# Kernel optimization log

Hardware: AMD Instinct MI355X
Metric: run time of the kernel (lower is better)

Reference implementation:

```python
import jax, jax.numpy as jnp
import numpy as np

D = 1024
H = 16
DK = D // H  # 64
CHUNK = 64
EPS = 1e-5


def setup_inputs() -> dict:
    key = jax.random.key(0)
    k1, k2, k3 = jax.random.split(key, 3)
    x = jax.random.normal(k1, (4, 4096, D), dtype=jnp.float32)
    W_qkv = jax.random.normal(k2, (D, 3 * D), dtype=jnp.float32) * 0.02
    W_o = jax.random.normal(k3, (D, D), dtype=jnp.float32) * 0.02
    return {"x": x, "W_qkv": W_qkv, "W_o": W_o}


def _layernorm_noaffine(k):
    mu = jnp.mean(k, axis=-1, keepdims=True)
    var = jnp.mean((k - mu) ** 2, axis=-1, keepdims=True)  # biased var, torch LayerNorm
    return (k - mu) / jnp.sqrt(var + EPS)


def _linear_attn(x, W_qkv, W_o):
    B, L, Dm = x.shape
    qkv = (x @ W_qkv).reshape(B, L, 3, H, DK)
    q, k, v = qkv[:, :, 0], qkv[:, :, 1], qkv[:, :, 2]
    k = _layernorm_noaffine(k)

    nC = L // CHUNK
    # [nC, B, C, H, DK] for scan over chunks
    to_chunks = lambda t: t.reshape(B, nC, CHUNK, H, DK).transpose(1, 0, 2, 3, 4)
    qc, kc, vc = to_chunks(q), to_chunks(k), to_chunks(v)

    causal = jnp.tril(jnp.ones((CHUNK, CHUNK), dtype=bool))  # s <= t inclusive

    def step(S, chunk):
        q_c, k_c, v_c = chunk  # each [B, C, H, DK]
        # inter-chunk: y_t += S_prev @ q_t
        inter = jnp.einsum('bhde,bthe->bthd', S, q_c)
        # intra-chunk: y_t += sum_{s<=t} (k_s . q_t) v_s
        scores = jnp.einsum('bthd,bshd->bhts', q_c, k_c)
        scores = jnp.where(causal, scores, 0.0)
        intra = jnp.einsum('bhts,bshd->bthd', scores, v_c)
        # state update: S += sum_t v_t k_t^T
        S = S + jnp.einsum('bthd,bthe->bhde', v_c, k_c)
        return S, inter + intra

    S0 = jnp.zeros((B, H, DK, DK), dtype=x.dtype)
    _, ys = jax.lax.scan(step, S0, (qc, kc, vc))  # ys: [nC, B, C, H, DK]
    y = ys.transpose(1, 0, 2, 3, 4).reshape(B, L, Dm)
    return y @ W_o


def reference(x, W_qkv, W_o):
    return _linear_attn(x, W_qkv, W_o)
```

## Files before the change

kernel.cpp:

```cpp
#include <hip/hip_runtime.h>

#define EPS 1e-5f

typedef __attribute__((ext_vector_type(8))) short s16x8;
typedef __attribute__((ext_vector_type(4))) float f4;

__device__ __forceinline__ short f2bf(float f) {
  union { float f; unsigned u; } x; x.f = f;
  unsigned r = x.u + 0x7fffu + ((x.u >> 16) & 1u);
  return (short)(r >> 16);
}
__device__ __forceinline__ float bf2f(short s) {
  union { unsigned u; float f; } x; x.u = ((unsigned)(unsigned short)s) << 16;
  return x.f;
}
__device__ __forceinline__ void gll16(const short* g, short* l) {
  __builtin_amdgcn_global_load_lds((const __attribute__((address_space(1))) void*)g,
                                   (__attribute__((address_space(3))) void*)l, 16, 0, 0);
}

#define BAR() asm volatile("s_barrier" ::: "memory")
#define LGKM0() do { asm volatile("s_waitcnt lgkmcnt(0)" ::: "memory"); \
                     __builtin_amdgcn_sched_barrier(0); } while (0)

__global__ __launch_bounds__(256) void prep(
    const float* __restrict__ x, const float* __restrict__ Wqkv,
    const float* __restrict__ Wo,
    short* __restrict__ xb, short* __restrict__ WqkvT, short* __restrict__ WoT)
{
  __shared__ float tile[32][33];
  const int bid = blockIdx.x;
  if (bid < 8192) {
    const size_t i = ((size_t)bid * 256 + threadIdx.x) * 8;
    const float4* p = reinterpret_cast<const float4*>(x + i);
    float4 a = p[0], b = p[1];
    union { uint4 v; short s[8]; } o;
    o.s[0] = f2bf(a.x); o.s[1] = f2bf(a.y); o.s[2] = f2bf(a.z); o.s[3] = f2bf(a.w);
    o.s[4] = f2bf(b.x); o.s[5] = f2bf(b.y); o.s[6] = f2bf(b.z); o.s[7] = f2bf(b.w);
    *reinterpret_cast<uint4*>(xb + i) = o.v;
    return;
  }
  const float* W; short* WT; int K, N, t;
  if (bid < 11264) { W = Wqkv; WT = WqkvT; K = 1024; N = 3072; t = bid - 8192;  }
  else             { W = Wo;   WT = WoT;   K = 1024; N = 1024; t = bid - 11264; }
  const int nblk = N >> 5;
  const int n0 = (t % nblk) * 32, k0 = (t / nblk) * 32;
  const int tx = threadIdx.x & 31, ty = threadIdx.x >> 5;
  #pragma unroll
  for (int i = 0; i < 4; i++) {
    int r = ty + i * 8;
    tile[r][tx] = W[(size_t)(k0 + r) * N + n0 + tx];
  }
  __syncthreads();
  #pragma unroll
  for (int i = 0; i < 4; i++) {
    int r = ty + i * 8;
    WT[(size_t)(n0 + r) * K + k0 + tx] = f2bf(tile[tx][r]);
  }
}

__device__ __forceinline__ void stage_slice(const short* __restrict__ G, short* dstbase,
                                            int row0, int kcol, int rowgrp, int panel, int lane) {
  short* dst = dstbase + panel * 8192 + rowgrp * 512;
  const short* src = G + (size_t)(row0 + rowgrp * 16 + (lane >> 2)) * 1024
                       + kcol + panel * 32 + (((lane & 3) << 3) ^ ((lane >> 5) << 4));
  gll16(src, dst);
}

template<bool STAGE>
__device__ __forceinline__ void ktile8p(
    const short* ldsAc, const short* ldsBc, short* ldsAn, short* ldsBn,
    const short* __restrict__ A, const short* __restrict__ BT,
    int m0, int n0, int knext,
    int w, int lane, int wm, int wn, int quad, int l16,
    f4 (&acc)[8][4])
{
  s16x8 bfr[4][2];
  const int co = (quad << 3) ^ ((l16 >> 3) << 4);
  #pragma unroll
  for (int p = 0; p < 4; ++p) {
    s16x8 a00, a01, a10, a11;
    {
      const int r0 = (wm * 128 + p * 32 + l16) * 32;
      a00 = *reinterpret_cast<const s16x8*>(&ldsAc[r0 + co]);
      a01 = *reinterpret_cast<const s16x8*>(&ldsAc[8192 + r0 + co]);
      a10 = *reinterpret_cast<const s16x8*>(&ldsAc[r0 + 512 + co]);
      a11 = *reinterpret_cast<const s16x8*>(&ldsAc[8192 + r0 + 512 + co]);
    }
    if (p == 0) {
      #pragma unroll
      for (int nf = 0; nf < 4; ++nf) {
        const int rb = (wn * 64 + nf * 16 + l16) * 32;
        bfr[nf][0] = *reinterpret_cast<const s16x8*>(&ldsBc[rb + co]);
        bfr[nf][1] = *reinterpret_cast<const s16x8*>(&ldsBc[8192 + rb + co]);
      }
    }
    if (STAGE) {
      if (p == 0)      { stage_slice(BT, ldsBn, n0, knext, w,     0, lane); stage_slice(BT, ldsBn, n0, knext, w,     1, lane); }
      else if (p == 1) { stage_slice(BT, ldsBn, n0, knext, 8 + w, 0, lane); stage_slice(BT, ldsBn, n0, knext, 8 + w, 1, lane); }
      else if (p == 2) { const int rg = (w & 3) + ((w >> 2) << 3);
                         stage_slice(A, ldsAn, m0, knext, rg, 0, lane); stage_slice(A, ldsAn, m0, knext, rg, 1, lane); }
      else             { const int rg = 4 + (w & 3) + ((w >> 2) << 3);
                         stage_slice(A, ldsAn, m0, knext, rg, 0, lane); stage_slice(A, ldsAn, m0, knext, rg, 1, lane); }
    }
    BAR();
    LGKM0();
    __builtin_amdgcn_s_setprio(1);
    #pragma unroll
    for (int nf = 0; nf < 4; ++nf) {
      acc[2*p  ][nf] = __builtin_amdgcn_mfma_f32_16x16x32_bf16(a00, bfr[nf][0], acc[2*p  ][nf], 0, 0, 0);
      acc[2*p  ][nf] = __builtin_amdgcn_mfma_f32_16x16x32_bf16(a01, bfr[nf][1], acc[2*p  ][nf], 0, 0, 0);
      acc[2*p+1][nf] = __builtin_amdgcn_mfma_f32_16x16x32_bf16(a10, bfr[nf][0], acc[2*p+1][nf], 0, 0, 0);
      acc[2*p+1][nf] = __builtin_amdgcn_mfma_f32_16x16x32_bf16(a11, bfr[nf][1], acc[2*p+1][nf], 0, 0, 0);
    }
    __builtin_amdgcn_s_setprio(0);
    if (p == 1) {
      if (STAGE) asm volatile("s_waitcnt vmcnt(4)" ::: "memory");
      else       asm volatile("s_waitcnt vmcnt(0)" ::: "memory");
    }
    if (p == 3 && STAGE) asm volatile("s_waitcnt vmcnt(2)" ::: "memory");
    BAR();
  }
}

#define GEMM8P_PROLOGUE()                                                            \
  stage_slice(BT, Bb0, n0, 0, w,     0, lane); stage_slice(BT, Bb0, n0, 0, w,     1, lane); \
  stage_slice(BT, Bb0, n0, 0, 8 + w, 0, lane); stage_slice(BT, Bb0, n0, 0, 8 + w, 1, lane); \
  { const int rg = (w & 3) + ((w >> 2) << 3);                                        \
    stage_slice(A, Ab0, m0, 0, rg, 0, lane); stage_slice(A, Ab0, m0, 0, rg, 1, lane); } \
  { const int rg = 4 + (w & 3) + ((w >> 2) << 3);                                    \
    stage_slice(A, Ab0, m0, 0, rg, 0, lane); stage_slice(A, Ab0, m0, 0, rg, 1, lane); } \
  asm volatile("s_waitcnt vmcnt(2)" ::: "memory");                                   \
  BAR()

#define GEMM8P_MAINLOOP()                                                            \
  _Pragma("unroll 1")                                                                \
  for (int t = 0; t < 14; t += 2) {                                                  \
    ktile8p<true>(Ab0, Bb0, Ab1, Bb1, A, BT, m0, n0, (t + 1) << 6, w, lane, wm, wn, quad, l16, acc); \
    ktile8p<true>(Ab1, Bb1, Ab0, Bb0, A, BT, m0, n0, (t + 2) << 6, w, lane, wm, wn, quad, l16, acc); \
  }                                                                                  \
  ktile8p<true >(Ab0, Bb0, Ab1, Bb1, A, BT, m0, n0, 15 << 6, w, lane, wm, wn, quad, l16, acc); \
  ktile8p<false>(Ab1, Bb1, Ab0, Bb0, A, BT, m0, n0, 0,       w, lane, wm, wn, quad, l16, acc)

__global__ __launch_bounds__(512, 2) void gemm_qkv_8p(
    const short* __restrict__ A, const short* __restrict__ BT,
    short* __restrict__ qb, short* __restrict__ kb, short* __restrict__ vb)
{
  extern __shared__ __align__(16) short lds[];
  short* Ab0 = lds;           short* Ab1 = lds + 16384;
  short* Bb0 = lds + 32768;   short* Bb1 = lds + 49152;

  const int pid = blockIdx.x;
  const int wg = (pid & 7) * 96 + (pid >> 3);
  const int mb = wg / 12, nb = wg % 12;
  const int m0 = mb * 256, n0 = nb * 256;

  const int tid = threadIdx.x;
  const int w = tid >> 6, lane = tid & 63, quad = lane >> 4, l16 = lane & 15;
  const int wm = w >> 2, wn = w & 3;

  f4 acc[8][4];
  #pragma unroll
  for (int i = 0; i < 8; i++)
    #pragma unroll
    for (int j = 0; j < 4; j++) acc[i][j] = {0.f, 0.f, 0.f, 0.f};

  GEMM8P_PROLOGUE();
  GEMM8P_MAINLOOP();

  __syncthreads();
  short* st = lds + w * 1152;
  const int j0 = n0 + wn * 64;
  const int sq = j0 >> 10;
  const int hh = (j0 >> 6) & 15;
  short* dbuf = (sq == 0) ? qb : (sq == 1) ? kb : vb;
  const int r2 = lane >> 3, c8 = (lane & 7) << 3;
  #pragma unroll
  for (int mf = 0; mf < 8; ++mf) {
    #pragma unroll
    for (int nf = 0; nf < 4; ++nf)
      #pragma unroll
      for (int r = 0; r < 4; ++r)
        st[(quad * 4 + r) * 72 + nf * 16 + l16] = f2bf(acc[mf][nf][r]);
    #pragma unroll
    for (int h2 = 0; h2 < 2; ++h2) {
      int rr = h2 * 8 + r2;
      int i = m0 + wm * 128 + mf * 16 + rr;
      int bb = i >> 12, ll = i & 4095;
      uint4 val = *reinterpret_cast<const uint4*>(&st[rr * 72 + c8]);
      *reinterpret_cast<uint4*>(&dbuf[(((size_t)(bb * 16 + hh)) * 4096 + ll) * 64 + c8]) = val;
    }
  }
}

__global__ __launch_bounds__(512, 2) void gemm_out_8p(
    const short* __restrict__ A, const short* __restrict__ BT, float* __restrict__ C)
{
  extern __shared__ __align__(16) short lds[];
  short* Ab0 = lds;           short* Ab1 = lds + 16384;
  short* Bb0 = lds + 32768;   short* Bb1 = lds + 49152;

  const int pid = blockIdx.x;
  const int wg = (pid & 7) * 32 + (pid >> 3);
  const int mb = wg >> 2, nb = wg & 3;
  const int m0 = mb * 256, n0 = nb * 256;

  const int tid = threadIdx.x;
  const int w = tid >> 6, lane = tid & 63, quad = lane >> 4, l16 = lane & 15;
  const int wm = w >> 2, wn = w & 3;

  f4 acc[8][4];
  #pragma unroll
  for (int i = 0; i < 8; i++)
    #pragma unroll
    for (int j = 0; j < 4; j++) acc[i][j] = {0.f, 0.f, 0.f, 0.f};

  GEMM8P_PROLOGUE();
  GEMM8P_MAINLOOP();

  #pragma unroll
  for (int mf = 0; mf < 8; ++mf)
    #pragma unroll
    for (int nf = 0; nf < 4; ++nf)
      #pragma unroll
      for (int r = 0; r < 4; ++r) {
        int i = m0 + wm * 128 + mf * 16 + quad * 4 + r;
        int j = n0 + wn * 64 + nf * 16 + l16;
        C[(size_t)i * 1024 + j] = acc[mf][nf][r];
      }
}

__global__ __launch_bounds__(256) void gemm_qkv_v4(
    const short* __restrict__ A, const short* __restrict__ BT,
    short* __restrict__ qb, short* __restrict__ kb, short* __restrict__ vb)
{
  __shared__ __align__(16) short lds[8192];
  short* As = lds;
  short* Bs = lds + 4096;

  const int p = blockIdx.x;
  const int slot = p >> 3;
  const int strip = (p & 7) + 8 * (slot / 24);
  const int nb = slot % 24;
  const int m0 = strip * 128, n0 = nb * 128;

  const int tid = threadIdx.x;
  const int w = tid >> 6, lane = tid & 63, quad = lane >> 4, l16 = lane & 15;
  const int wm = (w >> 1) << 6, wn = (w & 1) << 6;

  f4 acc[4][4];
  #pragma unroll
  for (int i = 0; i < 4; i++)
    #pragma unroll
    for (int j = 0; j < 4; j++) acc[i][j] = {0.f, 0.f, 0.f, 0.f};

  const int row = w * 32 + (lane >> 2), ofs = (lane & 3) << 3;

  for (int k0 = 0; k0 < 1024; k0 += 32) {
    __syncthreads();
    gll16(A + (size_t)(m0 + row) * 1024 + k0 + ofs, &As[(w * 32) * 32]);
    gll16(A + (size_t)(m0 + row + 16) * 1024 + k0 + ofs, &As[(w * 32 + 16) * 32]);
    gll16(BT + (size_t)(n0 + row) * 1024 + k0 + ofs, &Bs[(w * 32) * 32]);
    gll16(BT + (size_t)(n0 + row + 16) * 1024 + k0 + ofs, &Bs[(w * 32 + 16) * 32]);
    __syncthreads();
    s16x8 afr[4], bfr[4];
    #pragma unroll
    for (int t = 0; t < 4; t++)
      afr[t] = *reinterpret_cast<const s16x8*>(&As[(wm + t * 16 + l16) * 32 + quad * 8]);
    #pragma unroll
    for (int t = 0; t < 4; t++)
      bfr[t] = *reinterpret_cast<const s16x8*>(&Bs[(wn + t * 16 + l16) * 32 + quad * 8]);
    #pragma unroll
    for (int ti = 0; ti < 4; ti++)
      #pragma unroll
      for (int tj = 0; tj < 4; tj++)
        acc[ti][tj] = __builtin_amdgcn_mfma_f32_16x16x32_bf16(afr[ti], bfr[tj], acc[ti][tj], 0, 0, 0);
  }

  __syncthreads();
  short* st = &lds[w * 16 * 72];
  const int j0 = n0 + wn;
  const int sq = j0 >> 10;
  const int hh = (j0 >> 6) & 15;
  short* dbuf = (sq == 0) ? qb : (sq == 1) ? kb : vb;
  const int r2 = lane >> 3, c8 = (lane & 7) << 3;
  #pragma unroll
  for (int ti = 0; ti < 4; ti++) {
    #pragma unroll
    for (int tj = 0; tj < 4; tj++)
      #pragma unroll
      for (int r = 0; r < 4; r++)
        st[(quad * 4 + r) * 72 + tj * 16 + l16] = f2bf(acc[ti][tj][r]);
    #pragma unroll
    for (int h2 = 0; h2 < 2; h2++) {
      int rr = h2 * 8 + r2;
      int i = m0 + wm + ti * 16 + rr;
      int bb = i >> 12, ll = i & 4095;
      uint4 val = *reinterpret_cast<const uint4*>(&st[rr * 72 + c8]);
      *reinterpret_cast<uint4*>(&dbuf[(((size_t)(bb * 16 + hh)) * 4096 + ll) * 64 + c8]) = val;
    }
  }
}

__global__ __launch_bounds__(256) void ln_k(short* __restrict__ kbuf)
{
  const int row = blockIdx.x * 4 + (threadIdx.x >> 6);
  const int lane = threadIdx.x & 63;
  const size_t idx = (size_t)row * 64 + lane;
  float v = bf2f(kbuf[idx]);
  float s = v, s2 = v * v;
  #pragma unroll
  for (int off = 32; off; off >>= 1) {
    s += __shfl_xor(s, off);
    s2 += __shfl_xor(s2, off);
  }
  float mean = s * (1.f / 64.f);
  float var = s2 * (1.f / 64.f) - mean * mean;
  float rstd = rsqrtf(var + EPS);
  kbuf[idx] = f2bf((v - mean) * rstd);
}

__global__ __launch_bounds__(256) void chunk_outer(
    const short* __restrict__ kb, const short* __restrict__ vb,
    short* __restrict__ G)
{
  __shared__ __align__(16) short kT[64 * 72];
  __shared__ __align__(16) short vT[64 * 72];
  const int bh = blockIdx.x >> 6, c = blockIdx.x & 63;
  const int tid = threadIdx.x;
  const int w = tid >> 6, lane = tid & 63, quad = lane >> 4, l16 = lane & 15;
  const int srow = tid >> 2, sseg = (tid & 3) << 4;
  const size_t base = (size_t)bh * 262144 + (size_t)(c * 64 + srow) * 64 + sseg;

  {
    const float4* kp = reinterpret_cast<const float4*>(kb + base);
    union { float4 v[2]; short s[16]; } ku;
    ku.v[0] = kp[0]; ku.v[1] = kp[1];
    float kv[16]; float s = 0.f, s2 = 0.f;
    #pragma unroll
    for (int i = 0; i < 16; i++) { kv[i] = bf2f(ku.s[i]); s += kv[i]; s2 += kv[i] * kv[i]; }
    s += __shfl_xor(s, 1);  s2 += __shfl_xor(s2, 1);
    s += __shfl_xor(s, 2);  s2 += __shfl_xor(s2, 2);
    float mean = s * (1.f / 64.f);
    float var = s2 * (1.f / 64.f) - mean * mean;
    float rstd = rsqrtf(var + EPS);
    #pragma unroll
    for (int i = 0; i < 16; i++) kT[(sseg + i) * 72 + srow] = f2bf((kv[i] - mean) * rstd);
    const float4* vp = reinterpret_cast<const float4*>(vb + base);
    union { float4 v[2]; short s[16]; } vu;
    vu.v[0] = vp[0]; vu.v[1] = vp[1];
    #pragma unroll
    for (int i = 0; i < 16; i++) vT[(sseg + i) * 72 + srow] = vu.s[i];
  }
  __syncthreads();
  s16x8 va0 = *reinterpret_cast<const s16x8*>(&vT[(w * 16 + l16) * 72 + quad * 8]);
  s16x8 va1 = *reinterpret_cast<const s16x8*>(&vT[(w * 16 + l16) * 72 + 32 + quad * 8]);
  short* Gc = G + ((size_t)blockIdx.x) * 4096;
  #pragma unroll
  for (int tj = 0; tj < 4; tj++) {
    s16x8 kb0 = *reinterpret_cast<const s16x8*>(&kT[(tj * 16 + l16) * 72 + quad * 8]);
    s16x8 kb1 = *reinterpret_cast<const s16x8*>(&kT[(tj * 16 + l16) * 72 + 32 + quad * 8]);
    f4 z = {0.f, 0.f, 0.f, 0.f};
    z = __builtin_amdgcn_mfma_f32_16x16x32_bf16(va0, kb0, z, 0, 0, 0);
    z = __builtin_amdgcn_mfma_f32_16x16x32_bf16(va1, kb1, z, 0, 0, 0);
    #pragma unroll
    for (int r = 0; r < 4; r++)
      Gc[(w * 16 + quad * 4 + r) * 64 + tj * 16 + l16] = f2bf(z[r]);
  }
}

__global__ __launch_bounds__(128) void prefix_S(short* __restrict__ G)
{
  const int bh = blockIdx.x >> 3, rg = blockIdx.x & 7;
  const size_t base = (size_t)bh * 262144 + rg * 512 + threadIdx.x * 4;
  float s0 = 0.f, s1 = 0.f, s2 = 0.f, s3 = 0.f;
  for (int c = 0; c < 64; c++) {
    short* p = G + base + (size_t)c * 4096;
    union { uint2 v; short s[4]; } gu;
    gu.v = *reinterpret_cast<const uint2*>(p);
    float g0 = bf2f(gu.s[0]), g1 = bf2f(gu.s[1]), g2 = bf2f(gu.s[2]), g3 = bf2f(gu.s[3]);
    union { uint2 v; short s[4]; } su;
    su.s[0] = f2bf(s0); su.s[1] = f2bf(s1); su.s[2] = f2bf(s2); su.s[3] = f2bf(s3);
    *reinterpret_cast<uint2*>(p) = su.v;
    s0 += g0; s1 += g1; s2 += g2; s3 += g3;
  }
}

__global__ __launch_bounds__(256) void chunk_out(
    const short* __restrict__ qb, const short* __restrict__ kb,
    const short* __restrict__ vb, const short* __restrict__ S,
    short* __restrict__ yb)
{
  __shared__ __align__(16) short vT[64 * 72];
  __shared__ __align__(16) short Ps[64 * 72];
  const int bh = blockIdx.x >> 6, c = blockIdx.x & 63;
  const int b = bh >> 4, h = bh & 15;
  const int tid = threadIdx.x;
  const int w = tid >> 6, lane = tid & 63, quad = lane >> 4, l16 = lane & 15;
  const int srow = tid >> 2, sseg = (tid & 3) << 4;
  const size_t base = (size_t)bh * 262144 + (size_t)c * 4096;

  {
    const float4* vp = reinterpret_cast<const float4*>(vb + base + (size_t)srow * 64 + sseg);
    union { float4 v[2]; short s[16]; } vu;
    vu.v[0] = vp[0]; vu.v[1] = vp[1];
    #pragma unroll
    for (int i = 0; i < 16; i++) vT[(sseg + i) * 72 + srow] = vu.s[i];
  }
  s16x8 qa[4][2], kf[2], sf[2];
  #pragma unroll
  for (int ti = 0; ti < 4; ti++)
    #pragma unroll
    for (int kh = 0; kh < 2; kh++)
      qa[ti][kh] = *reinterpret_cast<const s16x8*>(
          qb + base + (size_t)(ti * 16 + l16) * 64 + kh * 32 + quad * 8);
  #pragma unroll
  for (int kh = 0; kh < 2; kh++) {
    kf[kh] = *reinterpret_cast<const s16x8*>(
        kb + base + (size_t)(w * 16 + l16) * 64 + kh * 32 + quad * 8);
    sf[kh] = *reinterpret_cast<const s16x8*>(
        S + base + (size_t)(w * 16 + l16) * 64 + kh * 32 + quad * 8);
  }
  {
    float kv[16]; float s = 0.f, s2 = 0.f;
    #pragma unroll
    for (int kh = 0; kh < 2; kh++)
      #pragma unroll
      for (int i = 0; i < 8; i++) {
        float f = bf2f(kf[kh][i]); kv[kh * 8 + i] = f; s += f; s2 += f * f;
      }
    s += __shfl_xor(s, 16);  s2 += __shfl_xor(s2, 16);
    s += __shfl_xor(s, 32);  s2 += __shfl_xor(s2, 32);
    float mean = s * (1.f / 64.f);
    float var = s2 * (1.f / 64.f) - mean * mean;
    float rstd = rsqrtf(var + EPS);
    #pragma unroll
    for (int kh = 0; kh < 2; kh++)
      #pragma unroll
      for (int i = 0; i < 8; i++)
        kf[kh][i] = f2bf((kv[kh * 8 + i] - mean) * rstd);
  }
  __syncthreads();
  #pragma unroll
  for (int ti = 0; ti < 4; ti++) {
    f4 z = {0.f, 0.f, 0.f, 0.f};
    z = __builtin_amdgcn_mfma_f32_16x16x32_bf16(qa[ti][0], kf[0], z, 0, 0, 0);
    z = __builtin_amdgcn_mfma_f32_16x16x32_bf16(qa[ti][1], kf[1], z, 0, 0, 0);
    #pragma unroll
    for (int r = 0; r < 4; r++) {
      int t = ti * 16 + quad * 4 + r;
      int s = w * 16 + l16;
      Ps[t * 72 + s] = (s <= t) ? f2bf(z[r]) : (short)0;
    }
  }
  __syncthreads();
  s16x8 vf0 = *reinterpret_cast<const s16x8*>(&vT[(w * 16 + l16) * 72 + quad * 8]);
  s16x8 vf1 = *reinterpret_cast<const s16x8*>(&vT[(w * 16 + l16) * 72 + 32 + quad * 8]);
  #pragma unroll
  for (int ti = 0; ti < 4; ti++) {
    f4 z = {0.f, 0.f, 0.f, 0.f};
    s16x8 p0 = *reinterpret_cast<const s16x8*>(&Ps[(ti * 16 + l16) * 72 + quad * 8]);
    s16x8 p1 = *reinterpret_cast<const s16x8*>(&Ps[(ti * 16 + l16) * 72 + 32 + quad * 8]);
    z = __builtin_amdgcn_mfma_f32_16x16x32_bf16(p0, vf0, z, 0, 0, 0);
    z = __builtin_amdgcn_mfma_f32_16x16x32_bf16(p1, vf1, z, 0, 0, 0);
    z = __builtin_amdgcn_mfma_f32_16x16x32_bf16(qa[ti][0], sf[0], z, 0, 0, 0);
    z = __builtin_amdgcn_mfma_f32_16x16x32_bf16(qa[ti][1], sf[1], z, 0, 0, 0);
    #pragma unroll
    for (int r = 0; r < 4; r++) {
      int t = ti * 16 + quad * 4 + r;
      int d = w * 16 + l16;
      yb[(((size_t)b * 4096) + c * 64 + t) * 1024 + h * 64 + d] = f2bf(z[r]);
    }
  }
}

__global__ __launch_bounds__(256) void gemm_out_v3(
    const short* __restrict__ A, const short* __restrict__ BT, float* __restrict__ C)
{
  __shared__ __align__(16) short As[128 * 32];
  __shared__ __align__(16) short Bs[128 * 32];
  const int p = blockIdx.x;
  const int slot = p >> 3;
  const int strip = (p & 7) + 8 * (slot >> 3);
  const int nb = slot & 7;
  const int m0 = strip * 128, n0 = nb * 128;
  const int tid = threadIdx.x;
  const int w = tid >> 6, lane = tid & 63, quad = lane >> 4, l16 = lane & 15;
  const int wm = (w >> 1) << 6, wn = (w & 1) << 6;

  f4 acc[4][4];
  #pragma unroll
  for (int i = 0; i < 4; i++)
    #pragma unroll
    for (int j = 0; j < 4; j++) acc[i][j] = {0.f, 0.f, 0.f, 0.f};

  const int row = w * 32 + (lane >> 2), ofs = (lane & 3) << 3;

  for (int k0 = 0; k0 < 1024; k0 += 32) {
    __syncthreads();
    gll16(A + (size_t)(m0 + row) * 1024 + k0 + ofs, &As[(w * 32) * 32]);
    gll16(A + (size_t)(m0 + row + 16) * 1024 + k0 + ofs, &As[(w * 32 + 16) * 32]);
    gll16(BT + (size_t)(n0 + row) * 1024 + k0 + ofs, &Bs[(w * 32) * 32]);
    gll16(BT + (size_t)(n0 + row + 16) * 1024 + k0 + ofs, &Bs[(w * 32 + 16) * 32]);
    __syncthreads();
    s16x8 afr[4], bfr[4];
    #pragma unroll
    for (int t = 0; t < 4; t++)
      afr[t] = *reinterpret_cast<const s16x8*>(&As[(wm + t * 16 + l16) * 32 + quad * 8]);
    #pragma unroll
    for (int t = 0; t < 4; t++)
      bfr[t] = *reinterpret_cast<const s16x8*>(&Bs[(wn + t * 16 + l16) * 32 + quad * 8]);
    #pragma unroll
    for (int ti = 0; ti < 4; ti++)
      #pragma unroll
      for (int tj = 0; tj < 4; tj++)
        acc[ti][tj] = __builtin_amdgcn_mfma_f32_16x16x32_bf16(afr[ti], bfr[tj], acc[ti][tj], 0, 0, 0);
  }
  #pragma unroll
  for (int ti = 0; ti < 4; ti++)
    #pragma unroll
    for (int tj = 0; tj < 4; tj++)
      #pragma unroll
      for (int r = 0; r < 4; r++) {
        int i = m0 + wm + ti * 16 + quad * 4 + r;
        int j = n0 + wn + tj * 16 + l16;
        C[(size_t)i * 1024 + j] = acc[ti][tj][r];
      }
}

__global__ __launch_bounds__(256) void gemm_qkv_r1(
    const float* __restrict__ A, const float* __restrict__ B,
    short* __restrict__ qb, short* __restrict__ kb, short* __restrict__ vb)
{
  __shared__ __align__(16) short As[128 * 40];
  __shared__ __align__(16) short Bs[128 * 40];
  const int n0 = blockIdx.x * 128;
  const int m0 = blockIdx.y * 128;
  const int tid = threadIdx.x;
  const int w = tid >> 6, lane = tid & 63, quad = lane >> 4, l16 = lane & 15;
  const int wm = (w >> 1) << 6, wn = (w & 1) << 6;
  f4 acc[4][4];
  #pragma unroll
  for (int i = 0; i < 4; i++)
    #pragma unroll
    for (int j = 0; j < 4; j++) acc[i][j] = {0.f, 0.f, 0.f, 0.f};
  const int arow = tid >> 1, aseg = (tid & 1) << 4;
  const int brow = tid >> 3, bseg = (tid & 7) << 4;
  for (int k0 = 0; k0 < 1024; k0 += 32) {
    __syncthreads();
    {
      const float4* ap = reinterpret_cast<const float4*>(A + (size_t)(m0 + arow) * 1024 + k0 + aseg);
      union { float4 v[4]; float f[16]; } af;
      af.v[0] = ap[0]; af.v[1] = ap[1]; af.v[2] = ap[2]; af.v[3] = ap[3];
      union { float4 v[2]; short s[16]; } ao;
      #pragma unroll
      for (int i = 0; i < 16; i++) ao.s[i] = f2bf(af.f[i]);
      float4* dst = reinterpret_cast<float4*>(&As[arow * 40 + aseg]);
      dst[0] = ao.v[0]; dst[1] = ao.v[1];
    }
    {
      const float4* bp = reinterpret_cast<const float4*>(B + (size_t)(k0 + brow) * 3072 + n0 + bseg);
      union { float4 v[4]; float f[16]; } bu;
      bu.v[0] = bp[0]; bu.v[1] = bp[1]; bu.v[2] = bp[2]; bu.v[3] = bp[3];
      #pragma unroll
      for (int i = 0; i < 16; i++) Bs[(bseg + i) * 40 + brow] = f2bf(bu.f[i]);
    }
    __syncthreads();
    s16x8 afr[4], bfr[4];
    #pragma unroll
    for (int t = 0; t < 4; t++)
      afr[t] = *reinterpret_cast<const s16x8*>(&As[(wm + t * 16 + l16) * 40 + quad * 8]);
    #pragma unroll
    for (int t = 0; t < 4; t++)
      bfr[t] = *reinterpret_cast<const s16x8*>(&Bs[(wn + t * 16 + l16) * 40 + quad * 8]);
    #pragma unroll
    for (int ti = 0; ti < 4; ti++)
      #pragma unroll
      for (int tj = 0; tj < 4; tj++)
        acc[ti][tj] = __builtin_amdgcn_mfma_f32_16x16x32_bf16(afr[ti], bfr[tj], acc[ti][tj], 0, 0, 0);
  }
  const int sq = n0 >> 10;
  short* dbuf = (sq == 0) ? qb : (sq == 1) ? kb : vb;
  #pragma unroll
  for (int ti = 0; ti < 4; ti++)
    #pragma unroll
    for (int tj = 0; tj < 4; tj++)
      #pragma unroll
      for (int r = 0; r < 4; r++) {
        int i = m0 + wm + ti * 16 + quad * 4 + r;
        int j = n0 + wn + tj * 16 + l16;
        int hh = (j >> 6) & 15, dd = j & 63;
        int bb = i >> 12, ll = i & 4095;
        dbuf[(((size_t)(bb * 16 + hh)) * 4096 + ll) * 64 + dd] = f2bf(acc[ti][tj][r]);
      }
}

__global__ __launch_bounds__(256) void scan_chunks_r1(
    const short* __restrict__ qb, const short* __restrict__ kb,
    const short* __restrict__ vb, short* __restrict__ yb)
{
  __shared__ __align__(16) short qs[64 * 72];
  __shared__ __align__(16) short ks[64 * 72];
  __shared__ __align__(16) short kT[64 * 72];
  __shared__ __align__(16) short vT[64 * 72];
  __shared__ __align__(16) short Sb[64 * 72];
  __shared__ __align__(16) short Ps[64 * 72];
  const int bh = blockIdx.x;
  const int b = bh >> 4, h = bh & 15;
  const int tid = threadIdx.x;
  const int w = tid >> 6, lane = tid & 63, quad = lane >> 4, l16 = lane & 15;
  const int srow = tid >> 2, sseg = (tid & 3) << 4;
  const size_t base = (size_t)bh * 4096 * 64;
  f4 accS[4];
  #pragma unroll
  for (int i = 0; i < 4; i++) accS[i] = {0.f, 0.f, 0.f, 0.f};
  for (int c = 0; c < 64; c++) {
    __syncthreads();
    {
      size_t g = base + ((size_t)(c * 64 + srow)) * 64 + sseg;
      const float4* qp = reinterpret_cast<const float4*>(qb + g);
      float4 q0 = qp[0], q1 = qp[1];
      *reinterpret_cast<float4*>(&qs[srow * 72 + sseg]) = q0;
      *reinterpret_cast<float4*>(&qs[srow * 72 + sseg + 8]) = q1;
      const float4* kp = reinterpret_cast<const float4*>(kb + g);
      union { float4 v[2]; short s[16]; } ku;
      ku.v[0] = kp[0]; ku.v[1] = kp[1];
      *reinterpret_cast<float4*>(&ks[srow * 72 + sseg]) = ku.v[0];
      *reinterpret_cast<float4*>(&ks[srow * 72 + sseg + 8]) = ku.v[1];
      #pragma unroll
      for (int i = 0; i < 16; i++) kT[(sseg + i) * 72 + srow] = ku.s[i];
      const float4* vp = reinterpret_cast<const float4*>(vb + g);
      union { float4 v[2]; short s[16]; } vu;
      vu.v[0] = vp[0]; vu.v[1] = vp[1];
      #pragma unroll
      for (int i = 0; i < 16; i++) vT[(sseg + i) * 72 + srow] = vu.s[i];
    }
    #pragma unroll
    for (int ti = 0; ti < 4; ti++)
      #pragma unroll
      for (int r = 0; r < 4; r++)
        Sb[(ti * 16 + quad * 4 + r) * 72 + w * 16 + l16] = f2bf(accS[ti][r]);
    __syncthreads();
    s16x8 qa[4][2];
    #pragma unroll
    for (int ti = 0; ti < 4; ti++)
      #pragma unroll
      for (int kh = 0; kh < 2; kh++)
        qa[ti][kh] = *reinterpret_cast<const s16x8*>(&qs[(ti * 16 + l16) * 72 + kh * 32 + quad * 8]);
    s16x8 kf[2];
    #pragma unroll
    for (int kh = 0; kh < 2; kh++)
      kf[kh] = *reinterpret_cast<const s16x8*>(&ks[(w * 16 + l16) * 72 + kh * 32 + quad * 8]);
    #pragma unroll
    for (int ti = 0; ti < 4; ti++) {
      f4 z = {0.f, 0.f, 0.f, 0.f};
      z = __builtin_amdgcn_mfma_f32_16x16x32_bf16(qa[ti][0], kf[0], z, 0, 0, 0);
      z = __builtin_amdgcn_mfma_f32_16x16x32_bf16(qa[ti][1], kf[1], z, 0, 0, 0);
      #pragma unroll
      for (int r = 0; r < 4; r++) {
        int t = ti * 16 + quad * 4 + r;
        int s = w * 16 + l16;
        Ps[t * 72 + s] = (s <= t) ? f2bf(z[r]) : (short)0;
      }
    }
    __syncthreads();
    s16x8 vf[2], sf[2];
    #pragma unroll
    for (int kh = 0; kh < 2; kh++) {
      vf[kh] = *reinterpret_cast<const s16x8*>(&vT[(w * 16 + l16) * 72 + kh * 32 + quad * 8]);
      sf[kh] = *reinterpret_cast<const s16x8*>(&Sb[(w * 16 + l16) * 72 + kh * 32 + quad * 8]);
    }
    #pragma unroll
    for (int ti = 0; ti < 4; ti++) {
      f4 z = {0.f, 0.f, 0.f, 0.f};
      s16x8 p0 = *reinterpret_cast<const s16x8*>(&Ps[(ti * 16 + l16) * 72 + quad * 8]);
      s16x8 p1 = *reinterpret_cast<const s16x8*>(&Ps[(ti * 16 + l16) * 72 + 32 + quad * 8]);
      z = __builtin_amdgcn_mfma_f32_16x16x32_bf16(p0, vf[0], z, 0, 0, 0);
      z = __builtin_amdgcn_mfma_f32_16x16x32_bf16(p1, vf[1], z, 0, 0, 0);
      z = __builtin_amdgcn_mfma_f32_16x16x32_bf16(qa[ti][0], sf[0], z, 0, 0, 0);
      z = __builtin_amdgcn_mfma_f32_16x16x32_bf16(qa[ti][1], sf[1], z, 0, 0, 0);
      #pragma unroll
      for (int r = 0; r < 4; r++) {
        int t = ti * 16 + quad * 4 + r;
        int d = w * 16 + l16;
        yb[(((size_t)b * 4096) + c * 64 + t) * 1024 + h * 64 + d] = f2bf(z[r]);
      }
    }
    s16x8 ku0 = *reinterpret_cast<const s16x8*>(&kT[(w * 16 + l16) * 72 + quad * 8]);
    s16x8 ku1 = *reinterpret_cast<const s16x8*>(&kT[(w * 16 + l16) * 72 + 32 + quad * 8]);
    #pragma unroll
    for (int ti = 0; ti < 4; ti++) {
      s16x8 va0 = *reinterpret_cast<const s16x8*>(&vT[(ti * 16 + l16) * 72 + quad * 8]);
      s16x8 va1 = *reinterpret_cast<const s16x8*>(&vT[(ti * 16 + l16) * 72 + 32 + quad * 8]);
      accS[ti] = __builtin_amdgcn_mfma_f32_16x16x32_bf16(va0, ku0, accS[ti], 0, 0, 0);
      accS[ti] = __builtin_amdgcn_mfma_f32_16x16x32_bf16(va1, ku1, accS[ti], 0, 0, 0);
    }
  }
}

__global__ __launch_bounds__(256) void gemm_out_r1(
    const short* __restrict__ A, const float* __restrict__ B, float* __restrict__ C)
{
  __shared__ __align__(16) short As[128 * 40];
  __shared__ __align__(16) short Bs[128 * 40];
  const int n0 = blockIdx.x * 128;
  const int m0 = blockIdx.y * 128;
  const int tid = threadIdx.x;
  const int w = tid >> 6, lane = tid & 63, quad = lane >> 4, l16 = lane & 15;
  const int wm = (w >> 1) << 6, wn = (w & 1) << 6;
  f4 acc[4][4];
  #pragma unroll
  for (int i = 0; i < 4; i++)
    #pragma unroll
    for (int j = 0; j < 4; j++) acc[i][j] = {0.f, 0.f, 0.f, 0.f};
  const int arow = tid >> 1, aseg = (tid & 1) << 4;
  const int brow = tid >> 3, bseg = (tid & 7) << 4;
  for (int k0 = 0; k0 < 1024; k0 += 32) {
    __syncthreads();
    {
      const float4* ap = reinterpret_cast<const float4*>(A + (size_t)(m0 + arow) * 1024 + k0 + aseg);
      float4 a0 = ap[0], a1 = ap[1];
      float4* dst = reinterpret_cast<float4*>(&As[arow * 40 + aseg]);
      dst[0] = a0; dst[1] = a1;
    }
    {
      const float4* bp = reinterpret_cast<const float4*>(B + (size_t)(k0 + brow) * 1024 + n0 + bseg);
      union { float4 v[4]; float f[16]; } bu;
      bu.v[0] = bp[0]; bu.v[1] = bp[1]; bu.v[2] = bp[2]; bu.v[3] = bp[3];
      #pragma unroll
      for (int i = 0; i < 16; i++) Bs[(bseg + i) * 40 + brow] = f2bf(bu.f[i]);
    }
    __syncthreads();
    s16x8 afr[4], bfr[4];
    #pragma unroll
    for (int t = 0; t < 4; t++)
      afr[t] = *reinterpret_cast<const s16x8*>(&As[(wm + t * 16 + l16) * 40 + quad * 8]);
    #pragma unroll
    for (int t = 0; t < 4; t++)
      bfr[t] = *reinterpret_cast<const s16x8*>(&Bs[(wn + t * 16 + l16) * 40 + quad * 8]);
    #pragma unroll
    for (int ti = 0; ti < 4; ti++)
      #pragma unroll
      for (int tj = 0; tj < 4; tj++)
        acc[ti][tj] = __builtin_amdgcn_mfma_f32_16x16x32_bf16(afr[ti], bfr[tj], acc[ti][tj], 0, 0, 0);
  }
  #pragma unroll
  for (int ti = 0; ti < 4; ti++)
    #pragma unroll
    for (int tj = 0; tj < 4; tj++)
      #pragma unroll
      for (int r = 0; r < 4; r++) {
        int i = m0 + wm + ti * 16 + quad * 4 + r;
        int j = n0 + wn + tj * 16 + l16;
        C[(size_t)i * 1024 + j] = acc[ti][tj][r];
      }
}

extern "C" void kernel_launch(void* const* d_in, const int* in_sizes, int n_in,
                              void* d_out, int out_size, void* d_ws, size_t ws_size,
                              hipStream_t stream) {
  const float* x    = (const float*)d_in[0];
  const float* Wqkv = (const float*)d_in[1];
  const float* Wo   = (const float*)d_in[2];
  float* out = (float*)d_out;

  short* qb = (short*)d_ws;
  short* kb = qb + (size_t)16777216;
  short* vb = kb + (size_t)16777216;
  short* yb = vb + (size_t)16777216;

  const size_t NEED = 176160768;
  if (ws_size >= NEED) {
    short* Gs    = yb + (size_t)16777216;
    short* WqkvT = Gs + (size_t)16777216;
    short* WoT   = WqkvT + (size_t)3145728;
    short* xb    = Gs;

    static int use8p = -1;
    if (use8p < 0) {
      hipError_t e1 = hipFuncSetAttribute((const void*)gemm_qkv_8p,
          hipFuncAttributeMaxDynamicSharedMemorySize, 131072);
      hipError_t e2 = hipFuncSetAttribute((const void*)gemm_out_8p,
          hipFuncAttributeMaxDynamicSharedMemorySize, 131072);
      use8p = (e1 == hipSuccess && e2 == hipSuccess) ? 1 : 0;
    }

    prep          <<<dim3(12288),   256, 0, stream>>>(x, Wqkv, Wo, xb, WqkvT, WoT);
    if (use8p)
      gemm_qkv_8p <<<dim3(768),     512, 131072, stream>>>(xb, WqkvT, qb, kb, vb);
    else
      gemm_qkv_v4 <<<dim3(3072),    256, 0, stream>>>(xb, WqkvT, qb, kb, vb);
    chunk_outer   <<<dim3(4096),    256, 0, stream>>>(kb, vb, Gs);
    prefix_S      <<<dim3(512),     128, 0, stream>>>(Gs);
    chunk_out     <<<dim3(4096),    256, 0, stream>>>(qb, kb, vb, Gs, yb);
    if (use8p)
      gemm_out_8p <<<dim3(256),     512, 131072, stream>>>(yb, WoT, out);
    else
      gemm_out_v3 <<<dim3(1024),    256, 0, stream>>>(yb, WoT, out);
  } else {
    gemm_qkv_r1   <<<dim3(24, 128), 256, 0, stream>>>(x, Wqkv, qb, kb, vb);
    ln_k          <<<dim3(65536),   256, 0, stream>>>(kb);
    scan_chunks_r1<<<dim3(64),      256, 0, stream>>>(qb, kb, vb, yb);
    gemm_out_r1   <<<dim3(8, 128),  256, 0, stream>>>(yb, Wo, out);
  }
}
```

Before: 315.1 us.

## XOR-swizzle transposed LDS tiles and prefetch next chunk in prefix scan

```diff
diff --git a/kernel.cpp b/kernel.cpp
--- a/kernel.cpp
+++ b/kernel.cpp
@@ -331,6 +331,7 @@
   const int w = tid >> 6, lane = tid & 63, quad = lane >> 4, l16 = lane & 15;
   const int srow = tid >> 2, sseg = (tid & 3) << 4;
   const size_t base = (size_t)bh * 262144 + (size_t)(c * 64 + srow) * 64 + sseg;
+  const int toff = ((((srow >> 3) ^ ((tid & 3) << 1)) & 7) << 3) + (srow & 7);
 
   {
     const float4* kp = reinterpret_cast<const float4*>(kb + base);
@@ -345,21 +346,23 @@
     float var = s2 * (1.f / 64.f) - mean * mean;
     float rstd = rsqrtf(var + EPS);
     #pragma unroll
-    for (int i = 0; i < 16; i++) kT[(sseg + i) * 72 + srow] = f2bf((kv[i] - mean) * rstd);
+    for (int i = 0; i < 16; i++) kT[(sseg + i) * 72 + toff] = f2bf((kv[i] - mean) * rstd);
     const float4* vp = reinterpret_cast<const float4*>(vb + base);
     union { float4 v[2]; short s[16]; } vu;
     vu.v[0] = vp[0]; vu.v[1] = vp[1];
     #pragma unroll
-    for (int i = 0; i < 16; i++) vT[(sseg + i) * 72 + srow] = vu.s[i];
+    for (int i = 0; i < 16; i++) vT[(sseg + i) * 72 + toff] = vu.s[i];
   }
   __syncthreads();
-  s16x8 va0 = *reinterpret_cast<const s16x8*>(&vT[(w * 16 + l16) * 72 + quad * 8]);
-  s16x8 va1 = *reinterpret_cast<const s16x8*>(&vT[(w * 16 + l16) * 72 + 32 + quad * 8]);
+  const int gsw = (w & 3) << 1;
+  s16x8 va0 = *reinterpret_cast<const s16x8*>(&vT[(w * 16 + l16) * 72 + ((quad ^ gsw) << 3)]);
+  s16x8 va1 = *reinterpret_cast<const s16x8*>(&vT[(w * 16 + l16) * 72 + (((4 + quad) ^ gsw) << 3)]);
   short* Gc = G + ((size_t)blockIdx.x) * 4096;
   #pragma unroll
   for (int tj = 0; tj < 4; tj++) {
-    s16x8 kb0 = *reinterpret_cast<const s16x8*>(&kT[(tj * 16 + l16) * 72 + quad * 8]);
-    s16x8 kb1 = *reinterpret_cast<const s16x8*>(&kT[(tj * 16 + l16) * 72 + 32 + quad * 8]);
+    const int gk = (tj & 3) << 1;
+    s16x8 kb0 = *reinterpret_cast<const s16x8*>(&kT[(tj * 16 + l16) * 72 + ((quad ^ gk) << 3)]);
+    s16x8 kb1 = *reinterpret_cast<const s16x8*>(&kT[(tj * 16 + l16) * 72 + (((4 + quad) ^ gk) << 3)]);
     f4 z = {0.f, 0.f, 0.f, 0.f};
     z = __builtin_amdgcn_mfma_f32_16x16x32_bf16(va0, kb0, z, 0, 0, 0);
     z = __builtin_amdgcn_mfma_f32_16x16x32_bf16(va1, kb1, z, 0, 0, 0);
@@ -372,17 +375,21 @@
 __global__ __launch_bounds__(128) void prefix_S(short* __restrict__ G)
 {
   const int bh = blockIdx.x >> 3, rg = blockIdx.x & 7;
-  const size_t base = (size_t)bh * 262144 + rg * 512 + threadIdx.x * 4;
+  short* p = G + (size_t)bh * 262144 + rg * 512 + threadIdx.x * 4;
   float s0 = 0.f, s1 = 0.f, s2 = 0.f, s3 = 0.f;
+  union U { uint2 v; short s[4]; };
+  U cur; cur.v = *reinterpret_cast<const uint2*>(p);
+  #pragma unroll 4
   for (int c = 0; c < 64; c++) {
-    short* p = G + base + (size_t)c * 4096;
-    union { uint2 v; short s[4]; } gu;
-    gu.v = *reinterpret_cast<const uint2*>(p);
-    float g0 = bf2f(gu.s[0]), g1 = bf2f(gu.s[1]), g2 = bf2f(gu.s[2]), g3 = bf2f(gu.s[3]);
-    union { uint2 v; short s[4]; } su;
+    short* pc = p + (size_t)c * 4096;
+    U nxt;
+    if (c < 63) nxt.v = *reinterpret_cast<const uint2*>(pc + 4096);
+    float g0 = bf2f(cur.s[0]), g1 = bf2f(cur.s[1]), g2 = bf2f(cur.s[2]), g3 = bf2f(cur.s[3]);
+    U su;
     su.s[0] = f2bf(s0); su.s[1] = f2bf(s1); su.s[2] = f2bf(s2); su.s[3] = f2bf(s3);
-    *reinterpret_cast<uint2*>(p) = su.v;
+    *reinterpret_cast<uint2*>(pc) = su.v;
     s0 += g0; s1 += g1; s2 += g2; s3 += g3;
+    cur = nxt;
   }
 }
 
@@ -399,13 +406,14 @@
   const int w = tid >> 6, lane = tid & 63, quad = lane >> 4, l16 = lane & 15;
   const int srow = tid >> 2, sseg = (tid & 3) << 4;
   const size_t base = (size_t)bh * 262144 + (size_t)c * 4096;
+  const int toff = ((((srow >> 3) ^ ((tid & 3) << 1)) & 7) << 3) + (srow & 7);
 
   {
     const float4* vp = reinterpret_cast<const float4*>(vb + base + (size_t)srow * 64 + sseg);
     union { float4 v[2]; short s[16]; } vu;
     vu.v[0] = vp[0]; vu.v[1] = vp[1];
     #pragma unroll
-    for (int i = 0; i < 16; i++) vT[(sseg + i) * 72 + srow] = vu.s[i];
+    for (int i = 0; i < 16; i++) vT[(sseg + i) * 72 + toff] = vu.s[i];
   }
   s16x8 qa[4][2], kf[2], sf[2];
   #pragma unroll
@@ -441,6 +449,7 @@
         kf[kh][i] = f2bf((kv[kh * 8 + i] - mean) * rstd);
   }
   __syncthreads();
+  const int psoff = ((((w * 16 + l16) >> 3) ^ (quad << 1)) << 3) + (l16 & 7);
   #pragma unroll
   for (int ti = 0; ti < 4; ti++) {
     f4 z = {0.f, 0.f, 0.f, 0.f};
@@ -450,17 +459,19 @@
     for (int r = 0; r < 4; r++) {
       int t = ti * 16 + quad * 4 + r;
       int s = w * 16 + l16;
-      Ps[t * 72 + s] = (s <= t) ? f2bf(z[r]) : (short)0;
+      Ps[t * 72 + psoff] = (s <= t) ? f2bf(z[r]) : (short)0;
     }
   }
   __syncthreads();
-  s16x8 vf0 = *reinterpret_cast<const s16x8*>(&vT[(w * 16 + l16) * 72 + quad * 8]);
-  s16x8 vf1 = *reinterpret_cast<const s16x8*>(&vT[(w * 16 + l16) * 72 + 32 + quad * 8]);
+  const int gsw = (w & 3) << 1;
+  s16x8 vf0 = *reinterpret_cast<const s16x8*>(&vT[(w * 16 + l16) * 72 + ((quad ^ gsw) << 3)]);
+  s16x8 vf1 = *reinterpret_cast<const s16x8*>(&vT[(w * 16 + l16) * 72 + (((4 + quad) ^ gsw) << 3)]);
+  const int pf = ((l16 >> 2) & 3) << 1;
   #pragma unroll
   for (int ti = 0; ti < 4; ti++) {
     f4 z = {0.f, 0.f, 0.f, 0.f};
-    s16x8 p0 = *reinterpret_cast<const s16x8*>(&Ps[(ti * 16 + l16) * 72 + quad * 8]);
-    s16x8 p1 = *reinterpret_cast<const s16x8*>(&Ps[(ti * 16 + l16) * 72 + 32 + quad * 8]);
+    s16x8 p0 = *reinterpret_cast<const s16x8*>(&Ps[(ti * 16 + l16) * 72 + ((quad ^ pf) << 3)]);
+    s16x8 p1 = *reinterpret_cast<const s16x8*>(&Ps[(ti * 16 + l16) * 72 + (((4 + quad) ^ pf) << 3)]);
     z = __builtin_amdgcn_mfma_f32_16x16x32_bf16(p0, vf0, z, 0, 0, 0);
     z = __builtin_amdgcn_mfma_f32_16x16x32_bf16(p1, vf1, z, 0, 0, 0);
     z = __builtin_amdgcn_mfma_f32_16x16x32_bf16(qa[ti][0], sf[0], z, 0, 0, 0);
```

New measurement: 321.1 us. About the same (+1.9%).
